# Kernel optimization log

Hardware: AMD Instinct MI355X
Metric: run time of the kernel (lower is better)

Reference implementation:

```python
import jax, jax.numpy as jnp
import numpy as np

NUM_EMBEDDINGS = 1024
EMBEDDING_DIM = 64
COMMITMENT_COST = 0.25


def setup_inputs() -> dict:
    key = jax.random.key(0)
    k1, k2 = jax.random.split(key)
    inputs = jax.random.normal(k1, (2, 64, 32, 32, 32), dtype=jnp.float32)
    embedding = jax.random.normal(k2, (NUM_EMBEDDINGS, EMBEDDING_DIM), dtype=jnp.float32)
    return {"inputs": inputs, "embedding": embedding}


def reference(inputs, embedding):
    # inputs: [B, C, D, H, W], embedding: [K, C]
    B, C, D, H, W = inputs.shape
    # flatten_permutation = [0, 2, 3, 4, 1] -> [B*D*H*W, C]
    flat_input = jnp.transpose(inputs, (0, 2, 3, 4, 1)).reshape(-1, C)
    # squared euclidean distances [N, K]
    distances = (
        jnp.sum(flat_input**2, axis=1, keepdims=True)
        + jnp.sum(embedding**2, axis=1)[None, :]
        - 2.0 * flat_input @ embedding.T
    )
    # torch.max(-distances, dim=1)[1] == argmin of distances
    encoding_indices = jnp.argmax(-distances, axis=1)  # [N]
    encoding_indices_view = encoding_indices.reshape(B, D, H, W)
    # embed: lookup then quantization_permutation [0, 4, 1, 2, 3] -> channel-first
    quantized = embedding[encoding_indices_view]            # [B, D, H, W, C]
    quantized = jnp.transpose(quantized, (0, 4, 1, 2, 3))   # [B, C, D, H, W]
    # commitment loss: MSE(stop_grad(quantized), inputs)
    loss = COMMITMENT_COST * jnp.mean((jax.lax.stop_gradient(quantized) - inputs) ** 2)
    # straight-through estimator
    quantized_st = inputs + jax.lax.stop_gradient(quantized - inputs)
    # eval path: encodings_sum = zeros(256) (hardcoded in original forward)
    encodings_sum = jnp.zeros(256, dtype=jnp.float32)
    return quantized_st, loss, encoding_indices_view, encodings_sum, embedding
```

## Files before the change

kernel.cpp:

```cpp
#include <hip/hip_runtime.h>
#include <stdint.h>

#define KCODES  1024
#define CDIM    64
#define SPATIAL 32768
#define NPOS    65536
#define NEL     4194304

#define OUT_Q    0
#define OUT_LOSS 4194304
#define OUT_IDX  4194305
#define OUT_SUM  4259841
#define OUT_EMB  4260097

#define REC_BYTES 33280
#define BPOS 64

typedef _Float16 half8 __attribute__((ext_vector_type(8)));
typedef float    f32x4 __attribute__((ext_vector_type(4)));

__global__ void prep_emb(const float* __restrict__ emb, char* __restrict__ ws,
                         float* __restrict__ out) {
    int gt = blockIdx.x * 256 + threadIdx.x;
    if (gt == 0) out[OUT_LOSS] = 0.f;
    if (gt < 256) out[OUT_SUM + gt] = 0.f;
    {
        float4 v = *(const float4*)(emb + (size_t)gt * 4);
        float* o = out + OUT_EMB + (size_t)gt * 4;
        o[0] = v.x; o[1] = v.y; o[2] = v.z; o[3] = v.w;
    }
    if (gt < 8192) {
        int k = gt >> 3, oct = gt & 7;
        int ch = k >> 7, mt = (k >> 4) & 7, row = k & 15;
        int s = oct >> 2, g = oct & 3;
        const float* e = emb + (size_t)k * CDIM + oct * 8;
        char* rec = ws + (size_t)ch * REC_BYTES;
        _Float16* hi = (_Float16*)rec + (size_t)(mt * 2 + s) * 512 + ((g << 4) | row) * 8;
        _Float16* lo = hi + 8192;
        float s2 = 0.f;
        half8 hv, lv;
#pragma unroll
        for (int i = 0; i < 8; ++i) {
            float v = e[i];
            s2 = fmaf(v, v, s2);
            _Float16 h = (_Float16)v;
            hv[i] = h;
            lv[i] = (_Float16)(v - (float)h);
        }
        *(half8*)hi = hv;
        *(half8*)lo = lv;
        s2 += __shfl_xor(s2, 1);
        s2 += __shfl_xor(s2, 2);
        s2 += __shfl_xor(s2, 4);
        if (oct == 0) ((float*)(rec + 32768))[k & 127] = -0.5f * s2;
    }
}

__global__ __launch_bounds__(256, 3) void vq_kernel(
        const float* __restrict__ in, const float* __restrict__ emb,
        const char* __restrict__ wsA, float* __restrict__ out) {
    __shared__ float xl[CDIM * 65];
    __shared__ float redS[4][4][16];
    __shared__ int   redK[4][4][16];
    __shared__ int   kwin[BPOS];

    const int tid  = threadIdx.x;
    const int lane = tid & 63, wv = tid >> 6;
    const int g = lane >> 4, col = lane & 15;
    const int p0 = blockIdx.x * BPOS;
    const int b  = p0 >> 15;
    const int s0 = p0 & 32767;
    const float* xin = in + (size_t)b * (CDIM * SPATIAL) + s0;

    {
        int p = tid & 63, cq = tid >> 6;
#pragma unroll
        for (int j = 0; j < 16; ++j) {
            int c = cq * 16 + j;
            xl[c * 65 + p] = xin[(size_t)c * SPATIAL + p];
        }
    }
    __syncthreads();

    half8 bh[4][2], bl[4][2];
#pragma unroll
    for (int t = 0; t < 4; ++t)
#pragma unroll
        for (int s = 0; s < 2; ++s) {
            int p = t * 16 + col;
#pragma unroll
            for (int i = 0; i < 8; ++i) {
                int c = s * 32 + g * 8 + i;
                float v = xl[c * 65 + p];
                _Float16 h = (_Float16)v;
                bh[t][s][i] = h;
                bl[t][s][i] = (_Float16)(v - (float)h);
            }
        }

    float best[4][4];
    int   bmt[4][4];
#pragma unroll
    for (int t = 0; t < 4; ++t)
#pragma unroll
        for (int r = 0; r < 4; ++r) { best[t][r] = -3.402823466e38f; bmt[t][r] = 0; }

    for (int o = 0; o < 4; ++o) {
#pragma unroll
        for (int ii = 0; ii < 4; ++ii) {
            int gmt = wv + 4 * (o * 4 + ii);
            const char* rec = wsA + (size_t)(gmt >> 3) * REC_BYTES;
            int mt = gmt & 7;
            const char* hp = rec + mt * 2048 + (size_t)lane * 16;
            half8 ah0 = *(const half8*)(hp);
            half8 ah1 = *(const half8*)(hp + 1024);
            half8 al0 = *(const half8*)(hp + 16384);
            half8 al1 = *(const half8*)(hp + 17408);
            f32x4 ei  = *(const f32x4*)(rec + 32768 + mt * 64 + g * 16);
#pragma unroll
            for (int t = 0; t < 4; ++t) {
                f32x4 a = ei;
                a = __builtin_amdgcn_mfma_f32_16x16x32_f16(ah0, bh[t][0], a, 0, 0, 0);
                a = __builtin_amdgcn_mfma_f32_16x16x32_f16(ah1, bh[t][1], a, 0, 0, 0);
                a = __builtin_amdgcn_mfma_f32_16x16x32_f16(ah0, bl[t][0], a, 0, 0, 0);
                a = __builtin_amdgcn_mfma_f32_16x16x32_f16(ah1, bl[t][1], a, 0, 0, 0);
                a = __builtin_amdgcn_mfma_f32_16x16x32_f16(al0, bh[t][0], a, 0, 0, 0);
                a = __builtin_amdgcn_mfma_f32_16x16x32_f16(al1, bh[t][1], a, 0, 0, 0);
#pragma unroll
                for (int r = 0; r < 4; ++r)
                    if (a[r] > best[t][r]) { best[t][r] = a[r]; bmt[t][r] = gmt; }
            }
        }
    }

#pragma unroll
    for (int t = 0; t < 4; ++t) {
        float bs = best[t][0];
        int   bk = bmt[t][0] * 16 + g * 4 + 0;
#pragma unroll
        for (int r = 1; r < 4; ++r) {
            float sc = best[t][r];
            int   k  = bmt[t][r] * 16 + g * 4 + r;
            if (sc > bs || (sc == bs && k < bk)) { bs = sc; bk = k; }
        }
#pragma unroll
        for (int m = 16; m <= 32; m <<= 1) {
            float os = __shfl_xor(bs, m);
            int   ok = __shfl_xor(bk, m);
            if (os > bs || (os == bs && ok < bk)) { bs = os; bk = ok; }
        }
        if (g == 0) { redS[wv][t][col] = bs; redK[wv][t][col] = bk; }
    }
    __syncthreads();

    if (wv == 0) {
        int t = lane >> 4, c2 = lane & 15;
        float bs = redS[0][t][c2];
        int   bk = redK[0][t][c2];
#pragma unroll
        for (int w = 1; w < 4; ++w) {
            float sc = redS[w][t][c2];
            int   k  = redK[w][t][c2];
            if (sc > bs || (sc == bs && k < bk)) { bs = sc; bk = k; }
        }
        kwin[lane] = bk;
        out[OUT_IDX + p0 + lane] = (float)bk;
    }
    __syncthreads();

    float lsum = 0.f;
    {
        int p = tid & 63, cq = tid >> 6;
        int kk = kwin[p];
        const float* eb = emb + (size_t)kk * CDIM;
        float* q = out + OUT_Q + (size_t)b * (CDIM * SPATIAL) + s0;
#pragma unroll
        for (int j = 0; j < 16; ++j) {
            int c = cq * 16 + j;
            float e = eb[c];
            float x = xl[c * 65 + p];
            float d = e - x;
            lsum = fmaf(d, d, lsum);
            q[(size_t)c * SPATIAL + p] = x + d;
        }
    }
#pragma unroll
    for (int off = 32; off > 0; off >>= 1) lsum += __shfl_down(lsum, off);
    if (lane == 0) redS[wv][0][0] = lsum;
    __syncthreads();
    if (tid == 0) {
        float t = redS[0][0][0] + redS[1][0][0] + redS[2][0][0] + redS[3][0][0];
        atomicAdd(out + OUT_LOSS, t * (0.25f / (float)NEL));
    }
}

extern "C" void kernel_launch(void* const* d_in, const int* in_sizes, int n_in,
                              void* d_out, int out_size, void* d_ws, size_t ws_size,
                              hipStream_t stream) {
    const float* in  = (const float*)d_in[0];
    const float* emb = (const float*)d_in[1];
    float* out = (float*)d_out;
    char*  ws  = (char*)d_ws;

    prep_emb<<<64, 256, 0, stream>>>(emb, ws, out);
    vq_kernel<<<NPOS / BPOS, 256, 0, stream>>>(in, emb, ws, out);
}
```

Before: 49.57 us.

## Double-buffer codebook tiles via global_load_lds into per-wave LDS staging

Codebook hi/lo fp16 fragments are no longer loaded straight into registers. Each wave now streams them with async global->LDS loads into a per-wave double buffer, prefetching the next tile while running MFMAs on the current one, with manual vmcnt waits. The aim is to hide global load latency in the distance loop. In exchange it adds 32KB of LDS, lowers the launch-bounds occupancy from 3 to 2, and relies on hand-counted vmcnt values, which are fragile and may also miss the LDS-write visibility.

```diff
diff --git a/kernel.cpp b/kernel.cpp
--- a/kernel.cpp
+++ b/kernel.cpp
@@ -56,9 +56,15 @@
     }
 }
 
-__global__ __launch_bounds__(256, 3) void vq_kernel(
+#define GLDS16(GSRC, LDST)                                                     \
+    __builtin_amdgcn_global_load_lds(                                          \
+        (const __attribute__((address_space(1))) void*)(GSRC),                 \
+        (__attribute__((address_space(3))) void*)(LDST), 16, 0, 0)
+
+__global__ __launch_bounds__(256, 2) void vq_kernel(
         const float* __restrict__ in, const float* __restrict__ emb,
         const char* __restrict__ wsA, float* __restrict__ out) {
+    __shared__ __align__(16) char stg[4][2][4096];
     __shared__ float xl[CDIM * 65];
     __shared__ float redS[4][4][16];
     __shared__ int   redK[4][4][16];
@@ -72,6 +78,27 @@
     const int s0 = p0 & 32767;
     const float* xin = in + (size_t)b * (CDIM * SPATIAL) + s0;
 
+    char* const sA = &stg[wv][0][0];
+    char* const sB = &stg[wv][1][0];
+
+#define STAGE(GMT, SB) do {                                                    \
+        int gmt_ = (GMT);                                                      \
+        const char* rec_ = wsA + (size_t)(gmt_ >> 3) * REC_BYTES;              \
+        int mt_ = gmt_ & 7;                                                    \
+        const char* h_ = rec_ + mt_ * 2048 + (size_t)lane * 16;                \
+        GLDS16(h_,         (SB));                                              \
+        GLDS16(h_ + 1024,  (SB) + 1024);                                       \
+        GLDS16(h_ + 16384, (SB) + 2048);                                       \
+        GLDS16(h_ + 17408, (SB) + 3072);                                       \
+    } while (0)
+
+#define LD_EI(GMT)                                                             \
+    (*(const f32x4*)(wsA + (size_t)((GMT) >> 3) * REC_BYTES + 32768 +          \
+                     ((GMT) & 7) * 64 + g * 16))
+
+    STAGE(wv, sA);
+    f32x4 eiA = LD_EI(wv);
+
     {
         int p = tid & 63, cq = tid >> 6;
 #pragma unroll
@@ -105,33 +132,49 @@
 #pragma unroll
         for (int r = 0; r < 4; ++r) { best[t][r] = -3.402823466e38f; bmt[t][r] = 0; }
 
-    for (int o = 0; o < 4; ++o) {
-#pragma unroll
-        for (int ii = 0; ii < 4; ++ii) {
-            int gmt = wv + 4 * (o * 4 + ii);
-            const char* rec = wsA + (size_t)(gmt >> 3) * REC_BYTES;
-            int mt = gmt & 7;
-            const char* hp = rec + mt * 2048 + (size_t)lane * 16;
-            half8 ah0 = *(const half8*)(hp);
-            half8 ah1 = *(const half8*)(hp + 1024);
-            half8 al0 = *(const half8*)(hp + 16384);
-            half8 al1 = *(const half8*)(hp + 17408);
-            f32x4 ei  = *(const f32x4*)(rec + 32768 + mt * 64 + g * 16);
-#pragma unroll
-            for (int t = 0; t < 4; ++t) {
-                f32x4 a = ei;
-                a = __builtin_amdgcn_mfma_f32_16x16x32_f16(ah0, bh[t][0], a, 0, 0, 0);
-                a = __builtin_amdgcn_mfma_f32_16x16x32_f16(ah1, bh[t][1], a, 0, 0, 0);
-                a = __builtin_amdgcn_mfma_f32_16x16x32_f16(ah0, bl[t][0], a, 0, 0, 0);
-                a = __builtin_amdgcn_mfma_f32_16x16x32_f16(ah1, bl[t][1], a, 0, 0, 0);
-                a = __builtin_amdgcn_mfma_f32_16x16x32_f16(al0, bh[t][0], a, 0, 0, 0);
-                a = __builtin_amdgcn_mfma_f32_16x16x32_f16(al1, bh[t][1], a, 0, 0, 0);
-#pragma unroll
-                for (int r = 0; r < 4; ++r)
-                    if (a[r] > best[t][r]) { best[t][r] = a[r]; bmt[t][r] = gmt; }
-            }
-        }
-    }
+#define CONSUME(SB, EI, GMT) do {                                              \
+        const char* sb_ = (SB) + (size_t)lane * 16;                            \
+        half8 ah0 = *(const half8*)(sb_);                                      \
+        half8 ah1 = *(const half8*)(sb_ + 1024);                               \
+        half8 al0 = *(const half8*)(sb_ + 2048);                               \
+        half8 al1 = *(const half8*)(sb_ + 3072);                               \
+        _Pragma("unroll")                                                      \
+        for (int t = 0; t < 4; ++t) {                                          \
+            f32x4 a = (EI);                                                    \
+            a = __builtin_amdgcn_mfma_f32_16x16x32_f16(ah0, bh[t][0], a, 0, 0, 0); \
+            a = __builtin_amdgcn_mfma_f32_16x16x32_f16(ah1, bh[t][1], a, 0, 0, 0); \
+            a = __builtin_amdgcn_mfma_f32_16x16x32_f16(ah0, bl[t][0], a, 0, 0, 0); \
+            a = __builtin_amdgcn_mfma_f32_16x16x32_f16(ah1, bl[t][1], a, 0, 0, 0); \
+            a = __builtin_amdgcn_mfma_f32_16x16x32_f16(al0, bh[t][0], a, 0, 0, 0); \
+            a = __builtin_amdgcn_mfma_f32_16x16x32_f16(al1, bh[t][1], a, 0, 0, 0); \
+            _Pragma("unroll")                                                  \
+            for (int r = 0; r < 4; ++r)                                        \
+                if (a[r] > best[t][r]) { best[t][r] = a[r]; bmt[t][r] = (GMT); } \
+        }                                                                      \
+    } while (0)
+
+#pragma unroll
+    for (int ii = 0; ii < 8; ++ii) {
+        const int gA = wv + 4 * (2 * ii);
+        const int gB = wv + 4 * (2 * ii + 1);
+        STAGE(gB, sB);
+        f32x4 eiB = LD_EI(gB);
+        asm volatile("s_waitcnt vmcnt(5)" ::: "memory");
+        CONSUME(sA, eiA, gA);
+        if (ii < 7) {
+            const int gN = wv + 4 * (2 * ii + 2);
+            STAGE(gN, sA);
+            eiA = LD_EI(gN);
+            asm volatile("s_waitcnt vmcnt(5)" ::: "memory");
+        } else {
+            asm volatile("s_waitcnt vmcnt(0)" ::: "memory");
+        }
+        CONSUME(sB, eiB, gB);
+    }
+#undef STAGE
+#undef LD_EI
+#undef CONSUME
+#undef GLDS16
 
 #pragma unroll
     for (int t = 0; t < 4; ++t) {
```

After: 70.01 us. +41.2%, slower.

## Stream codebook through double-buffered LDS with 32x32 MFMA and larger blocks

Applied to the files above, without the earlier changes.

Restructures the VQ kernel so each 512-thread block handles 256 positions. The fp16 hi/lo codebook is streamed in 32-code sets through a double-buffered LDS staging area using global_load_lds, replacing per-wave global loads. The distance MFMAs switch from 16x16x32 to 32x32x16, so each wave holds one 32-position tile and the cross-wave argmin reduction shrinks. The epilogue re-reads the inputs from global memory instead of keeping them in LDS. The cost is fewer blocks (256), a barrier after every set, and extra global reads in the epilogue. Ties in the per-lane argmin are now resolved by scan order rather than by explicit index comparison.

```diff
diff --git a/kernel.cpp b/kernel.cpp
--- a/kernel.cpp
+++ b/kernel.cpp
@@ -13,11 +13,14 @@
 #define OUT_SUM  4259841
 #define OUT_EMB  4260097
 
-#define REC_BYTES 33280
-#define BPOS 64
-
-typedef _Float16 half8 __attribute__((ext_vector_type(8)));
-typedef float    f32x4 __attribute__((ext_vector_type(4)));
+#define NSET  32
+#define SETB  8192
+#define EIOFF 262144
+#define BPOS  256
+
+typedef _Float16 half8  __attribute__((ext_vector_type(8)));
+typedef float    f32x4  __attribute__((ext_vector_type(4)));
+typedef float    f32x16 __attribute__((ext_vector_type(16)));
 
 __global__ void prep_emb(const float* __restrict__ emb, char* __restrict__ ws,
                          float* __restrict__ out) {
@@ -31,12 +34,12 @@
     }
     if (gt < 8192) {
         int k = gt >> 3, oct = gt & 7;
-        int ch = k >> 7, mt = (k >> 4) & 7, row = k & 15;
-        int s = oct >> 2, g = oct & 3;
+        int set = k >> 5, row = k & 31;
+        int ks = oct >> 1, hc = oct & 1;
         const float* e = emb + (size_t)k * CDIM + oct * 8;
-        char* rec = ws + (size_t)ch * REC_BYTES;
-        _Float16* hi = (_Float16*)rec + (size_t)(mt * 2 + s) * 512 + ((g << 4) | row) * 8;
-        _Float16* lo = hi + 8192;
+        char* rec = ws + (size_t)set * SETB;
+        _Float16* hi = (_Float16*)(rec + (ks * 2 + 0) * 1024 + (hc * 32 + row) * 16);
+        _Float16* lo = (_Float16*)(rec + (ks * 2 + 1) * 1024 + (hc * 32 + row) * 16);
         float s2 = 0.f;
         half8 hv, lv;
 #pragma unroll
@@ -52,133 +55,129 @@
         s2 += __shfl_xor(s2, 1);
         s2 += __shfl_xor(s2, 2);
         s2 += __shfl_xor(s2, 4);
-        if (oct == 0) ((float*)(rec + 32768))[k & 127] = -0.5f * s2;
+        if (oct == 0) ((float*)(ws + EIOFF))[k] = -0.5f * s2;
     }
 }
 
-__global__ __launch_bounds__(256, 3) void vq_kernel(
+#define GLDS16(GSRC, LDST)                                                     \
+    __builtin_amdgcn_global_load_lds(                                          \
+        (const __attribute__((address_space(1))) void*)(GSRC),                 \
+        (__attribute__((address_space(3))) void*)(LDST), 16, 0, 0)
+
+__global__ __launch_bounds__(512, 2) void vq_kernel(
         const float* __restrict__ in, const float* __restrict__ emb,
         const char* __restrict__ wsA, float* __restrict__ out) {
-    __shared__ float xl[CDIM * 65];
-    __shared__ float redS[4][4][16];
-    __shared__ int   redK[4][4][16];
+    __shared__ __align__(16) char stg[2][SETB];
+    __shared__ float xl[CDIM * 129];
     __shared__ int   kwin[BPOS];
+    __shared__ float lred[8];
 
     const int tid  = threadIdx.x;
     const int lane = tid & 63, wv = tid >> 6;
-    const int g = lane >> 4, col = lane & 15;
-    const int p0 = blockIdx.x * BPOS;
-    const int b  = p0 >> 15;
-    const int s0 = p0 & 32767;
+    const int col  = lane & 31, h = lane >> 5;
+    const int p0   = blockIdx.x * BPOS;
+    const int b    = p0 >> 15;
+    const int s0   = p0 & 32767;
     const float* xin = in + (size_t)b * (CDIM * SPATIAL) + s0;
+    const float* eiG = (const float*)(wsA + EIOFF);
+
+    GLDS16(wsA + (size_t)wv * 1024 + lane * 16, &stg[0][0] + wv * 1024 + lane * 16);
+
+    half8 bh[4], bl[4];
+    for (int H = 0; H < 2; ++H) {
+        {
+            int p = tid & 127, cq = tid >> 7;
+#pragma unroll
+            for (int j = 0; j < 16; ++j) {
+                int c = cq * 16 + j;
+                xl[c * 129 + p] = xin[(size_t)c * SPATIAL + H * 128 + p];
+            }
+        }
+        __syncthreads();
+        if ((wv >> 2) == H) {
+            int pp = (wv & 3) * 32 + col;
+#pragma unroll
+            for (int ks = 0; ks < 4; ++ks)
+#pragma unroll
+                for (int j = 0; j < 8; ++j) {
+                    int c = ks * 16 + h * 8 + j;
+                    float v = xl[c * 129 + pp];
+                    _Float16 hh = (_Float16)v;
+                    bh[ks][j] = hh;
+                    bl[ks][j] = (_Float16)(v - (float)hh);
+                }
+        }
+        if (H == 0) {
+            __syncthreads();
+        } else {
+            asm volatile("s_waitcnt vmcnt(0)" ::: "memory");
+            __syncthreads();
+        }
+    }
+
+    float best = -3.402823466e38f;
+    int   bk   = 0;
+#pragma unroll 2
+    for (int it = 0; it < NSET; ++it) {
+        char* cur = &stg[0][0] + (size_t)(it & 1) * SETB;
+        if (it + 1 < NSET) {
+            char* nxt = &stg[0][0] + (size_t)((it + 1) & 1) * SETB;
+            GLDS16(wsA + (size_t)(it + 1) * SETB + wv * 1024 + lane * 16,
+                   nxt + wv * 1024 + lane * 16);
+        }
+        f32x4 ei0 = *(const f32x4*)(eiG + it * 32 + 0 * 8 + 4 * h);
+        f32x4 ei1 = *(const f32x4*)(eiG + it * 32 + 1 * 8 + 4 * h);
+        f32x4 ei2 = *(const f32x4*)(eiG + it * 32 + 2 * 8 + 4 * h);
+        f32x4 ei3 = *(const f32x4*)(eiG + it * 32 + 3 * 8 + 4 * h);
+
+        f32x16 acc;
+#pragma unroll
+        for (int q = 0; q < 16; ++q) acc[q] = 0.f;
+        const char* ap = cur + (size_t)lane * 16;
+#pragma unroll
+        for (int ks = 0; ks < 4; ++ks) {
+            half8 ah = *(const half8*)(ap + (ks * 2 + 0) * 1024);
+            half8 al = *(const half8*)(ap + (ks * 2 + 1) * 1024);
+            acc = __builtin_amdgcn_mfma_f32_32x32x16_f16(ah, bh[ks], acc, 0, 0, 0);
+            acc = __builtin_amdgcn_mfma_f32_32x32x16_f16(ah, bl[ks], acc, 0, 0, 0);
+            acc = __builtin_amdgcn_mfma_f32_32x32x16_f16(al, bh[ks], acc, 0, 0, 0);
+        }
+        int kb = it * 32 + 4 * h;
+#pragma unroll
+        for (int m = 0; m < 4; ++m) {
+            f32x4 ev = (m == 0) ? ei0 : (m == 1) ? ei1 : (m == 2) ? ei2 : ei3;
+#pragma unroll
+            for (int r = 0; r < 4; ++r) {
+                float sc = acc[m * 4 + r] + ev[r];
+                if (sc > best) { best = sc; bk = kb + m * 8 + r; }
+            }
+        }
+        asm volatile("s_waitcnt vmcnt(0)" ::: "memory");
+        __syncthreads();
+    }
 
     {
-        int p = tid & 63, cq = tid >> 6;
-#pragma unroll
-        for (int j = 0; j < 16; ++j) {
-            int c = cq * 16 + j;
-            xl[c * 65 + p] = xin[(size_t)c * SPATIAL + p];
-        }
-    }
-    __syncthreads();
-
-    half8 bh[4][2], bl[4][2];
-#pragma unroll
-    for (int t = 0; t < 4; ++t)
-#pragma unroll
-        for (int s = 0; s < 2; ++s) {
-            int p = t * 16 + col;
-#pragma unroll
-            for (int i = 0; i < 8; ++i) {
-                int c = s * 32 + g * 8 + i;
-                float v = xl[c * 65 + p];
-                _Float16 h = (_Float16)v;
-                bh[t][s][i] = h;
-                bl[t][s][i] = (_Float16)(v - (float)h);
-            }
-        }
-
-    float best[4][4];
-    int   bmt[4][4];
-#pragma unroll
-    for (int t = 0; t < 4; ++t)
-#pragma unroll
-        for (int r = 0; r < 4; ++r) { best[t][r] = -3.402823466e38f; bmt[t][r] = 0; }
-
-    for (int o = 0; o < 4; ++o) {
-#pragma unroll
-        for (int ii = 0; ii < 4; ++ii) {
-            int gmt = wv + 4 * (o * 4 + ii);
-            const char* rec = wsA + (size_t)(gmt >> 3) * REC_BYTES;
-            int mt = gmt & 7;
-            const char* hp = rec + mt * 2048 + (size_t)lane * 16;
-            half8 ah0 = *(const half8*)(hp);
-            half8 ah1 = *(const half8*)(hp + 1024);
-            half8 al0 = *(const half8*)(hp + 16384);
-            half8 al1 = *(const half8*)(hp + 17408);
-            f32x4 ei  = *(const f32x4*)(rec + 32768 + mt * 64 + g * 16);
-#pragma unroll
-            for (int t = 0; t < 4; ++t) {
-                f32x4 a = ei;
-                a = __builtin_amdgcn_mfma_f32_16x16x32_f16(ah0, bh[t][0], a, 0, 0, 0);
-                a = __builtin_amdgcn_mfma_f32_16x16x32_f16(ah1, bh[t][1], a, 0, 0, 0);
-                a = __builtin_amdgcn_mfma_f32_16x16x32_f16(ah0, bl[t][0], a, 0, 0, 0);
-                a = __builtin_amdgcn_mfma_f32_16x16x32_f16(ah1, bl[t][1], a, 0, 0, 0);
-                a = __builtin_amdgcn_mfma_f32_16x16x32_f16(al0, bh[t][0], a, 0, 0, 0);
-                a = __builtin_amdgcn_mfma_f32_16x16x32_f16(al1, bh[t][1], a, 0, 0, 0);
-#pragma unroll
-                for (int r = 0; r < 4; ++r)
-                    if (a[r] > best[t][r]) { best[t][r] = a[r]; bmt[t][r] = gmt; }
-            }
-        }
-    }
-
-#pragma unroll
-    for (int t = 0; t < 4; ++t) {
-        float bs = best[t][0];
-        int   bk = bmt[t][0] * 16 + g * 4 + 0;
-#pragma unroll
-        for (int r = 1; r < 4; ++r) {
-            float sc = best[t][r];
-            int   k  = bmt[t][r] * 16 + g * 4 + r;
-            if (sc > bs || (sc == bs && k < bk)) { bs = sc; bk = k; }
-        }
-#pragma unroll
-        for (int m = 16; m <= 32; m <<= 1) {
-            float os = __shfl_xor(bs, m);
-            int   ok = __shfl_xor(bk, m);
-            if (os > bs || (os == bs && ok < bk)) { bs = os; bk = ok; }
-        }
-        if (g == 0) { redS[wv][t][col] = bs; redK[wv][t][col] = bk; }
-    }
-    __syncthreads();
-
-    if (wv == 0) {
-        int t = lane >> 4, c2 = lane & 15;
-        float bs = redS[0][t][c2];
-        int   bk = redK[0][t][c2];
-#pragma unroll
-        for (int w = 1; w < 4; ++w) {
-            float sc = redS[w][t][c2];
-            int   k  = redK[w][t][c2];
-            if (sc > bs || (sc == bs && k < bk)) { bs = sc; bk = k; }
-        }
-        kwin[lane] = bk;
-        out[OUT_IDX + p0 + lane] = (float)bk;
+        float os = __shfl_xor(best, 32);
+        int   ok = __shfl_xor(bk, 32);
+        if (os > best || (os == best && ok < bk)) { best = os; bk = ok; }
+        if (lane < 32) {
+            kwin[wv * 32 + col] = bk;
+            out[OUT_IDX + p0 + wv * 32 + col] = (float)bk;
+        }
     }
     __syncthreads();
 
     float lsum = 0.f;
     {
-        int p = tid & 63, cq = tid >> 6;
+        int p = tid & 255, cq = tid >> 8;
         int kk = kwin[p];
         const float* eb = emb + (size_t)kk * CDIM;
         float* q = out + OUT_Q + (size_t)b * (CDIM * SPATIAL) + s0;
 #pragma unroll
-        for (int j = 0; j < 16; ++j) {
-            int c = cq * 16 + j;
+        for (int j = 0; j < 32; ++j) {
+            int c = cq * 32 + j;
+            float x = xin[(size_t)c * SPATIAL + p];
             float e = eb[c];
-            float x = xl[c * 65 + p];
             float d = e - x;
             lsum = fmaf(d, d, lsum);
             q[(size_t)c * SPATIAL + p] = x + d;
@@ -186,10 +185,12 @@
     }
 #pragma unroll
     for (int off = 32; off > 0; off >>= 1) lsum += __shfl_down(lsum, off);
-    if (lane == 0) redS[wv][0][0] = lsum;
+    if (lane == 0) lred[wv] = lsum;
     __syncthreads();
     if (tid == 0) {
-        float t = redS[0][0][0] + redS[1][0][0] + redS[2][0][0] + redS[3][0][0];
+        float t = 0.f;
+#pragma unroll
+        for (int w = 0; w < 8; ++w) t += lred[w];
         atomicAdd(out + OUT_LOSS, t * (0.25f / (float)NEL));
     }
 }
@@ -203,5 +204,5 @@
     char*  ws  = (char*)d_ws;
 
     prep_emb<<<64, 256, 0, stream>>>(emb, ws, out);
-    vq_kernel<<<NPOS / BPOS, 256, 0, stream>>>(in, emb, ws, out);
+    vq_kernel<<<NPOS / BPOS, 512, 0, stream>>>(in, emb, ws, out);
 }
```

Measured after the change: 50.15 us. Within noise of the previous version (+1.2%).
